# Kernel tuning notes

Hardware: AMD Instinct MI355X
Metric: run time of the kernel (lower is better)

## Reference

```python
import jax, jax.numpy as jnp
import numpy as np

N, P, E, HID = 20000, 12, 640000, 100

def setup_inputs() -> dict:
    key = jax.random.key(0)
    ks = jax.random.split(key, 20)
    inp = {}
    inp['x'] = jax.random.normal(ks[0], (N, P), dtype=jnp.float32)
    inp['edge_index'] = jax.random.randint(ks[1], (2, E), 0, N, dtype=jnp.int64)
    inp['edge_weight'] = jax.random.uniform(ks[2], (E,), dtype=jnp.float32)
    s = 0.1
    # GCNConv weights (in=1, out=HID) and biases for z, r, h gates
    inp['W_z'] = jax.random.normal(ks[3], (1, HID)) * s
    inp['b_z'] = jnp.zeros((HID,))
    inp['W_r'] = jax.random.normal(ks[4], (1, HID)) * s
    inp['b_r'] = jnp.zeros((HID,))
    inp['W_h'] = jax.random.normal(ks[5], (1, HID)) * s
    inp['b_h'] = jnp.zeros((HID,))
    # TGCN linear layers: Linear(2*HID, HID), stored as (in, out)
    inp['Wl_z'] = jax.random.normal(ks[6], (2 * HID, HID)) * s
    inp['bl_z'] = jnp.zeros((HID,))
    inp['Wl_r'] = jax.random.normal(ks[7], (2 * HID, HID)) * s
    inp['bl_r'] = jnp.zeros((HID,))
    inp['Wl_h'] = jax.random.normal(ks[8], (2 * HID, HID)) * s
    inp['bl_h'] = jnp.zeros((HID,))
    # A3TGCN temporal attention logits over periods
    inp['att'] = jax.random.uniform(ks[9], (P,))
    # final Linear(100, 1)
    inp['W_out'] = jax.random.normal(ks[10], (HID, 1)) * s
    inp['b_out'] = jnp.zeros((1,))
    return inp

def _gcn_aggregate(x_np, edge_index, edge_weight):
    # symmetric GCN normalization with self-loops (PyG gcn_norm), then
    # aggregate neighbor features: out[i] = sum_j norm_ij * x[j]
    n = x_np.shape[0]
    src, dst = edge_index[0], edge_index[1]
    loop = jnp.arange(n)
    s = jnp.concatenate([src, loop])
    d = jnp.concatenate([dst, loop])
    w = jnp.concatenate([edge_weight, jnp.ones((n,), dtype=x_np.dtype)])
    deg = jax.ops.segment_sum(w, d, num_segments=n)
    dinv = jnp.where(deg > 0, deg ** -0.5, 0.0)
    norm = dinv[s] * w * dinv[d]                      # (E+N,)
    msgs = norm[:, None] * x_np[s]                    # (E+N, P)
    return jax.ops.segment_sum(msgs, d, num_segments=n)  # (N, P)

def reference(x, edge_index, edge_weight, W_z, b_z, W_r, b_r, W_h, b_h,
              Wl_z, bl_z, Wl_r, bl_r, Wl_h, bl_h, att, W_out, b_out):
    # x: (N, P) -> viewed as (N, in_channels=1, P) in the torch module.
    # GCNConv is linear in x, so aggregate once and apply each gate's weight.
    agg = _gcn_aggregate(x, edge_index, edge_weight)       # (N, P)
    C_z = agg[:, :, None] * W_z[0] + b_z                   # (N, P, HID)
    C_r = agg[:, :, None] * W_r[0] + b_r
    C_h = agg[:, :, None] * W_h[0] + b_h
    # A3TGCN calls TGCN with H=None (zeros) for every period independently.
    H0 = jnp.zeros_like(C_z)
    Z = jax.nn.sigmoid(jnp.concatenate([C_z, H0], -1) @ Wl_z + bl_z)
    R = jax.nn.sigmoid(jnp.concatenate([C_r, H0], -1) @ Wl_r + bl_r)
    Ht = jnp.tanh(jnp.concatenate([C_h, H0 * R], -1) @ Wl_h + bl_h)
    Hp = Z * H0 + (1.0 - Z) * Ht                           # (N, P, HID)
    probs = jax.nn.softmax(att)                            # (P,)
    H_acc = jnp.einsum('npo,p->no', Hp, probs)             # (N, HID)
    h = jax.nn.relu(H_acc)
    return h @ W_out + b_out                               # (N, 1)
```

## Files before the change

kernel.cpp:

```cpp
#include <hip/hip_runtime.h>
#include <hip/hip_bf16.h>

constexpr int N_NODES = 20000;
constexpr int P_PER   = 12;
constexpr int N_EDGES = 640000;
constexpr int HID     = 100;

constexpr int BIN_W   = 64;
constexpr int NB      = (N_NODES + BIN_W - 1) / BIN_W;
constexpr int BCAP    = 2560;
constexpr int NBLK2   = 320;
constexpr int CHUNK   = N_EDGES / NBLK2;
constexpr int CUR_STR = 16;
constexpr int Y_STR   = 16;
constexpr int GL      = 8;

constexpr size_t OFF_DINV  = 0;
constexpr size_t OFF_UZ    = OFF_DINV + N_NODES;
constexpr size_t OFF_CZ    = OFF_UZ + HID;
constexpr size_t OFF_UH    = OFF_CZ + HID;
constexpr size_t OFF_CH    = OFF_UH + HID;
constexpr size_t OFF_PROBS = OFF_CH + HID;
constexpr size_t OFF_CUR   = 20416;
constexpr size_t OFF_Y     = OFF_CUR + (size_t)NB * CUR_STR;
constexpr size_t OFF_SEG   = OFF_Y + (size_t)N_NODES * Y_STR;
constexpr size_t OFF_SEG2  = OFF_SEG + (size_t)NB * BCAP * 2;
constexpr size_t OFF_ROW   = OFF_SEG2 + (size_t)NB * BCAP * 2;

__global__ __launch_bounds__(256) void precompute_kernel(
        const float* __restrict__ Wz, const float* __restrict__ bz,
        const float* __restrict__ Wh, const float* __restrict__ bh,
        const float* __restrict__ Wlz, const float* __restrict__ blz,
        const float* __restrict__ Wlh, const float* __restrict__ blh,
        const float* __restrict__ att,
        float* __restrict__ uz, float* __restrict__ cz,
        float* __restrict__ uh, float* __restrict__ ch,
        float* __restrict__ probs, int* __restrict__ cur) {
    int t = threadIdx.x;
    for (int i = t; i < NB * CUR_STR; i += 256) cur[i] = 0;
    if (t < HID) {
        float suz = 0.f, scz = 0.f, suh = 0.f, sch = 0.f;
        for (int j = 0; j < HID; ++j) {
            float wlz = Wlz[j * HID + t];
            float wlh = Wlh[j * HID + t];
            suz += Wz[j] * wlz;
            scz += bz[j] * wlz;
            suh += Wh[j] * wlh;
            sch += bh[j] * wlh;
        }
        uz[t] = suz;
        cz[t] = scz + blz[t];
        uh[t] = suh;
        ch[t] = sch + blh[t];
    }
    if (t == 0) {
        float m = att[0];
        for (int p = 1; p < P_PER; ++p) m = fmaxf(m, att[p]);
        float e[P_PER];
        float s = 0.f;
        for (int p = 0; p < P_PER; ++p) { e[p] = __expf(att[p] - m); s += e[p]; }
        float inv = 1.0f / s;
        for (int p = 0; p < P_PER; ++p) probs[p] = e[p] * inv;
    }
}

__global__ __launch_bounds__(256) void partition_kernel(const int* __restrict__ ei,
                                                        const float* __restrict__ w,
                                                        int* __restrict__ cur,
                                                        int2* __restrict__ seg) {
    __shared__ int hist[NB];
    __shared__ int base[NB];
    __shared__ int run[NB];
    int t = threadIdx.x;
    for (int b = t; b < NB; b += 256) { hist[b] = 0; run[b] = 0; }
    __syncthreads();
    int e0 = blockIdx.x * CHUNK;
    const int* __restrict__ dsts = ei + N_EDGES;
    for (int i = t; i < CHUNK; i += 256) {
        int d = dsts[e0 + i];
        atomicAdd(&hist[d >> 6], 1);
    }
    __syncthreads();
    for (int b = t; b < NB; b += 256) {
        int h = hist[b];
        base[b] = (h > 0) ? atomicAdd(cur + (size_t)b * CUR_STR, h) : 0;
    }
    __syncthreads();
    for (int i = t; i < CHUNK; i += 256) {
        int s = ei[e0 + i];
        int d = dsts[e0 + i];
        float wt = w[e0 + i];
        int b = d >> 6;
        int pos = base[b] + atomicAdd(&run[b], 1);
        if (pos < BCAP)
            seg[(size_t)b * BCAP + pos] = make_int2(s | ((d & 63) << 16), __float_as_int(wt));
    }
}

__global__ __launch_bounds__(256) void binsort_kernel(const int2* __restrict__ seg,
                                                      const int* __restrict__ cur,
                                                      const float* __restrict__ x,
                                                      float* __restrict__ y,
                                                      int2* __restrict__ seg2,
                                                      int4* __restrict__ rowinfo) {
    __shared__ int2 ent2[BCAP];
    __shared__ int  hist[BIN_W];
    __shared__ int  off[BIN_W];
    __shared__ int  excl[BIN_W];
    __shared__ float sdinv[BIN_W];
    int t = threadIdx.x;
    int b = blockIdx.x;
    if (t < BIN_W) hist[t] = 0;
    __syncthreads();
    int c = min(cur[(size_t)b * CUR_STR], BCAP);
    const int2* sg = seg + (size_t)b * BCAP;
    for (int i = t; i < c; i += 256) atomicAdd(&hist[sg[i].x >> 16], 1);
    __syncthreads();
    if (t < 64) {
        int v = hist[t];
        int inc = v;
#pragma unroll
        for (int o = 1; o < 64; o <<= 1) {
            int u = __shfl_up(inc, o, 64);
            if (t >= o) inc += u;
        }
        int ex = inc - v;
        excl[t] = ex;
        off[t]  = ex;
    }
    __syncthreads();
    for (int i = t; i < c; i += 256) {
        int2 e = sg[i];
        int dl = e.x >> 16;
        int p = atomicAdd(&off[dl], 1);
        ent2[p] = make_int2(e.x & 0xFFFF, e.y);
    }
    __syncthreads();
    {
        int nl = t >> 2, l = t & 3;
        int beg = excl[nl];
        int end = beg + hist[nl];
        float s = 0.f;
        for (int j = beg + l; j < end; j += 4) s += __int_as_float(ent2[j].y);
        s += __shfl_xor(s, 1, 64);
        s += __shfl_xor(s, 2, 64);
        if (l == 0) sdinv[nl] = rsqrtf(1.0f + s);
    }
    __syncthreads();
    int n0 = b * BIN_W;
    int2* s2 = seg2 + (size_t)b * BCAP;
    for (int i = t; i < c; i += 256) s2[i] = ent2[i];
    if (t < BIN_W && n0 + t < N_NODES)
        rowinfo[n0 + t] = make_int4(b * BCAP + excl[t], hist[t],
                                    __float_as_int(sdinv[t]), 0);
    for (int i = t; i < BIN_W * P_PER; i += 256) {
        int nl = i / P_PER, p = i - nl * P_PER;
        int n = n0 + nl;
        if (n < N_NODES) y[(size_t)n * Y_STR + p] = sdinv[nl] * x[(size_t)n * P_PER + p];
    }
}

__global__ __launch_bounds__(256) void gather_finalize_kernel(const int2* __restrict__ seg2,
                                                              const int4* __restrict__ rowinfo,
                                                              const float* __restrict__ y,
                                                              const float* __restrict__ uz,
                                                              const float* __restrict__ cz,
                                                              const float* __restrict__ uh,
                                                              const float* __restrict__ ch,
                                                              const float* __restrict__ probs,
                                                              const float* __restrict__ Wout,
                                                              const float* __restrict__ bout,
                                                              float* __restrict__ out) {
    __shared__ float s_uz[HID], s_cz[HID], s_uh[HID], s_ch[HID], s_wo[HID];
    __shared__ float s_pr[P_PER];
    int t = threadIdx.x;
    if (t < HID) {
        s_uz[t] = uz[t]; s_cz[t] = cz[t];
        s_uh[t] = uh[t]; s_ch[t] = ch[t];
        s_wo[t] = Wout[t];
    }
    if (t < P_PER) s_pr[t] = probs[t];
    __syncthreads();

    int tid = blockIdx.x * blockDim.x + t;
    int n = tid >> 3;
    int l = tid & (GL - 1);
    if (n >= N_NODES) return;

    int4 ri = rowinfo[n];
    float acc[P_PER];
#pragma unroll
    for (int p = 0; p < P_PER; ++p) acc[p] = 0.f;
    int end = ri.x + ri.y;
    for (int j = ri.x + l; j < end; j += GL) {
        int2 e = seg2[j];
        float wt = __int_as_float(e.y);
        const float4* yr = (const float4*)(y + (size_t)e.x * Y_STR);
        float4 y0 = yr[0], y1 = yr[1], y2 = yr[2];
        acc[0]  += wt * y0.x;  acc[1]  += wt * y0.y;
        acc[2]  += wt * y0.z;  acc[3]  += wt * y0.w;
        acc[4]  += wt * y1.x;  acc[5]  += wt * y1.y;
        acc[6]  += wt * y1.z;  acc[7]  += wt * y1.w;
        acc[8]  += wt * y2.x;  acc[9]  += wt * y2.y;
        acc[10] += wt * y2.z;  acc[11] += wt * y2.w;
    }
#pragma unroll
    for (int off = 4; off >= 1; off >>= 1) {
#pragma unroll
        for (int p = 0; p < P_PER; ++p) acc[p] += __shfl_xor(acc[p], off, 64);
    }
    {
        float dn = __int_as_float(ri.z);
        const float4* yr = (const float4*)(y + (size_t)n * Y_STR);
        float4 y0 = yr[0], y1 = yr[1], y2 = yr[2];
        acc[0]  = dn * (acc[0]  + y0.x);  acc[1]  = dn * (acc[1]  + y0.y);
        acc[2]  = dn * (acc[2]  + y0.z);  acc[3]  = dn * (acc[3]  + y0.w);
        acc[4]  = dn * (acc[4]  + y1.x);  acc[5]  = dn * (acc[5]  + y1.y);
        acc[6]  = dn * (acc[6]  + y1.z);  acc[7]  = dn * (acc[7]  + y1.w);
        acc[8]  = dn * (acc[8]  + y2.x);  acc[9]  = dn * (acc[9]  + y2.y);
        acc[10] = dn * (acc[10] + y2.z);  acc[11] = dn * (acc[11] + y2.w);
    }
    float rk = 0.f;
    for (int k = l; k < HID; k += GL) {
        float uzk = s_uz[k], czk = s_cz[k], uhk = s_uh[k], chk = s_ch[k];
        float a2 = 0.f;
#pragma unroll
        for (int p = 0; p < P_PER; ++p) {
            float av = acc[p];
            float vz = fminf(fmaxf(av * uzk + czk, -30.f), 30.f);
            float vh = fminf(fmaxf(av * uhk + chk, -15.f), 15.f);
            float ez  = __expf(vz);
            float e2h = __expf(2.0f * vh);
            float term = (e2h - 1.0f) / ((1.0f + ez) * (e2h + 1.0f));
            a2 += s_pr[p] * term;
        }
        rk += fmaxf(a2, 0.0f) * s_wo[k];
    }
#pragma unroll
    for (int off = 4; off >= 1; off >>= 1) rk += __shfl_xor(rk, off, 64);
    if (l == 0) out[n] = rk + bout[0];
}

extern "C" void kernel_launch(void* const* d_in, const int* in_sizes, int n_in,
                              void* d_out, int out_size, void* d_ws, size_t ws_size,
                              hipStream_t stream) {
    const float* x   = (const float*)d_in[0];
    const int*   ei  = (const int*)d_in[1];
    const float* ew  = (const float*)d_in[2];
    const float* Wz  = (const float*)d_in[3];
    const float* bz  = (const float*)d_in[4];
    const float* Wh  = (const float*)d_in[7];
    const float* bh  = (const float*)d_in[8];
    const float* Wlz = (const float*)d_in[9];
    const float* blz = (const float*)d_in[10];
    const float* Wlh = (const float*)d_in[13];
    const float* blh = (const float*)d_in[14];
    const float* att = (const float*)d_in[15];
    const float* Wout = (const float*)d_in[16];
    const float* bout = (const float*)d_in[17];
    float* out = (float*)d_out;

    float* ws      = (float*)d_ws;
    float* uz      = ws + OFF_UZ;
    float* cz      = ws + OFF_CZ;
    float* uh      = ws + OFF_UH;
    float* ch      = ws + OFF_CH;
    float* probs   = ws + OFF_PROBS;
    int*   cur     = (int*)(ws + OFF_CUR);
    float* y       = ws + OFF_Y;
    int2*  seg     = (int2*)(ws + OFF_SEG);
    int2*  seg2    = (int2*)(ws + OFF_SEG2);
    int4*  rowinfo = (int4*)(ws + OFF_ROW);

    hipLaunchKernelGGL(precompute_kernel, dim3(1), dim3(256), 0, stream,
                       Wz, bz, Wh, bh, Wlz, blz, Wlh, blh, att, uz, cz, uh, ch, probs, cur);
    hipLaunchKernelGGL(partition_kernel, dim3(NBLK2), dim3(256), 0, stream,
                       ei, ew, cur, seg);
    hipLaunchKernelGGL(binsort_kernel, dim3(NB), dim3(256), 0, stream,
                       seg, cur, x, y, seg2, rowinfo);
    hipLaunchKernelGGL(gather_finalize_kernel, dim3((N_NODES * GL + 255) / 256), dim3(256), 0, stream,
                       seg2, rowinfo, y, uz, cz, uh, ch, probs, Wout, bout, out);
}
```

Baseline: 157.4 us.

## Fuse partition, binsort and gather into one cooperative grid-synced kernel

```diff
diff --git a/kernel.cpp b/kernel.cpp
--- a/kernel.cpp
+++ b/kernel.cpp
@@ -1,199 +1,176 @@
 #include <hip/hip_runtime.h>
 #include <hip/hip_bf16.h>
+#include <hip/hip_cooperative_groups.h>
+
+namespace cg = cooperative_groups;
 
 constexpr int N_NODES = 20000;
 constexpr int P_PER   = 12;
 constexpr int N_EDGES = 640000;
 constexpr int HID     = 100;
 
-constexpr int BIN_W   = 64;
-constexpr int NB      = (N_NODES + BIN_W - 1) / BIN_W;
-constexpr int BCAP    = 2560;
-constexpr int NBLK2   = 320;
-constexpr int CHUNK   = N_EDGES / NBLK2;
-constexpr int CUR_STR = 16;
-constexpr int Y_STR   = 16;
-constexpr int GL      = 8;
-
-constexpr size_t OFF_DINV  = 0;
-constexpr size_t OFF_UZ    = OFF_DINV + N_NODES;
+constexpr int BIN_W  = 64;
+constexpr int NB     = (N_NODES + BIN_W - 1) / BIN_W;
+constexpr int GRID   = 512;
+constexpr int TPB    = 256;
+constexpr int PCHUNK = N_EDGES / GRID;
+constexpr int SCAP   = 20;
+constexpr int ECAP   = 2560;
+constexpr int Y_STR  = 16;
+
+constexpr size_t OFF_UZ    = 0;
 constexpr size_t OFF_CZ    = OFF_UZ + HID;
 constexpr size_t OFF_UH    = OFF_CZ + HID;
 constexpr size_t OFF_CH    = OFF_UH + HID;
 constexpr size_t OFF_PROBS = OFF_CH + HID;
-constexpr size_t OFF_CUR   = 20416;
-constexpr size_t OFF_Y     = OFF_CUR + (size_t)NB * CUR_STR;
+constexpr size_t OFF_COUNT = 416;
+constexpr size_t OFF_Y     = OFF_COUNT + (size_t)GRID * NB;
 constexpr size_t OFF_SEG   = OFF_Y + (size_t)N_NODES * Y_STR;
-constexpr size_t OFF_SEG2  = OFF_SEG + (size_t)NB * BCAP * 2;
-constexpr size_t OFF_ROW   = OFF_SEG2 + (size_t)NB * BCAP * 2;
-
-__global__ __launch_bounds__(256) void precompute_kernel(
+
+__global__ __launch_bounds__(TPB) void fused_kernel(
+        const float* __restrict__ x, const int* __restrict__ ei, const float* __restrict__ ew,
         const float* __restrict__ Wz, const float* __restrict__ bz,
         const float* __restrict__ Wh, const float* __restrict__ bh,
         const float* __restrict__ Wlz, const float* __restrict__ blz,
         const float* __restrict__ Wlh, const float* __restrict__ blh,
-        const float* __restrict__ att,
-        float* __restrict__ uz, float* __restrict__ cz,
-        float* __restrict__ uh, float* __restrict__ ch,
-        float* __restrict__ probs, int* __restrict__ cur) {
-    int t = threadIdx.x;
-    for (int i = t; i < NB * CUR_STR; i += 256) cur[i] = 0;
-    if (t < HID) {
-        float suz = 0.f, scz = 0.f, suh = 0.f, sch = 0.f;
-        for (int j = 0; j < HID; ++j) {
-            float wlz = Wlz[j * HID + t];
-            float wlh = Wlh[j * HID + t];
-            suz += Wz[j] * wlz;
-            scz += bz[j] * wlz;
-            suh += Wh[j] * wlh;
-            sch += bh[j] * wlh;
-        }
-        uz[t] = suz;
-        cz[t] = scz + blz[t];
-        uh[t] = suh;
-        ch[t] = sch + blh[t];
-    }
-    if (t == 0) {
-        float m = att[0];
-        for (int p = 1; p < P_PER; ++p) m = fmaxf(m, att[p]);
-        float e[P_PER];
-        float s = 0.f;
-        for (int p = 0; p < P_PER; ++p) { e[p] = __expf(att[p] - m); s += e[p]; }
-        float inv = 1.0f / s;
-        for (int p = 0; p < P_PER; ++p) probs[p] = e[p] * inv;
-    }
-}
-
-__global__ __launch_bounds__(256) void partition_kernel(const int* __restrict__ ei,
-                                                        const float* __restrict__ w,
-                                                        int* __restrict__ cur,
-                                                        int2* __restrict__ seg) {
-    __shared__ int hist[NB];
-    __shared__ int base[NB];
-    __shared__ int run[NB];
-    int t = threadIdx.x;
-    for (int b = t; b < NB; b += 256) { hist[b] = 0; run[b] = 0; }
-    __syncthreads();
-    int e0 = blockIdx.x * CHUNK;
-    const int* __restrict__ dsts = ei + N_EDGES;
-    for (int i = t; i < CHUNK; i += 256) {
-        int d = dsts[e0 + i];
-        atomicAdd(&hist[d >> 6], 1);
-    }
-    __syncthreads();
-    for (int b = t; b < NB; b += 256) {
-        int h = hist[b];
-        base[b] = (h > 0) ? atomicAdd(cur + (size_t)b * CUR_STR, h) : 0;
-    }
-    __syncthreads();
-    for (int i = t; i < CHUNK; i += 256) {
-        int s = ei[e0 + i];
-        int d = dsts[e0 + i];
-        float wt = w[e0 + i];
-        int b = d >> 6;
-        int pos = base[b] + atomicAdd(&run[b], 1);
-        if (pos < BCAP)
-            seg[(size_t)b * BCAP + pos] = make_int2(s | ((d & 63) << 16), __float_as_int(wt));
-    }
-}
-
-__global__ __launch_bounds__(256) void binsort_kernel(const int2* __restrict__ seg,
-                                                      const int* __restrict__ cur,
-                                                      const float* __restrict__ x,
-                                                      float* __restrict__ y,
-                                                      int2* __restrict__ seg2,
-                                                      int4* __restrict__ rowinfo) {
-    __shared__ int2 ent2[BCAP];
-    __shared__ int  hist[BIN_W];
-    __shared__ int  off[BIN_W];
-    __shared__ int  excl[BIN_W];
+        const float* __restrict__ att, const float* __restrict__ Wout,
+        const float* __restrict__ bout, float* __restrict__ out,
+        float* __restrict__ uzg, float* __restrict__ czg,
+        float* __restrict__ uhg, float* __restrict__ chg, float* __restrict__ probsg,
+        int* __restrict__ count, float* __restrict__ y, int2* __restrict__ seg) {
+    cg::grid_group grid = cg::this_grid();
+
+    __shared__ int   run[NB];
+    __shared__ int   scnt[GRID];
+    __shared__ int2  ent2[ECAP];
+    __shared__ int   nhist[BIN_W], nexcl[BIN_W], noff[BIN_W];
     __shared__ float sdinv[BIN_W];
-    int t = threadIdx.x;
-    int b = blockIdx.x;
-    if (t < BIN_W) hist[t] = 0;
-    __syncthreads();
-    int c = min(cur[(size_t)b * CUR_STR], BCAP);
-    const int2* sg = seg + (size_t)b * BCAP;
-    for (int i = t; i < c; i += 256) atomicAdd(&hist[sg[i].x >> 16], 1);
-    __syncthreads();
-    if (t < 64) {
-        int v = hist[t];
-        int inc = v;
-#pragma unroll
-        for (int o = 1; o < 64; o <<= 1) {
-            int u = __shfl_up(inc, o, 64);
-            if (t >= o) inc += u;
-        }
-        int ex = inc - v;
-        excl[t] = ex;
-        off[t]  = ex;
-    }
-    __syncthreads();
-    for (int i = t; i < c; i += 256) {
-        int2 e = sg[i];
-        int dl = e.x >> 16;
-        int p = atomicAdd(&off[dl], 1);
-        ent2[p] = make_int2(e.x & 0xFFFF, e.y);
-    }
+    __shared__ float s_uz[HID], s_cz[HID], s_uh[HID], s_ch[HID], s_wo[HID];
+    __shared__ float s_pr[P_PER];
+
+    const int t   = threadIdx.x;
+    const int blk = blockIdx.x;
+
+    for (int b = t; b < NB; b += TPB) run[b] = 0;
     __syncthreads();
     {
-        int nl = t >> 2, l = t & 3;
-        int beg = excl[nl];
-        int end = beg + hist[nl];
-        float s = 0.f;
-        for (int j = beg + l; j < end; j += 4) s += __int_as_float(ent2[j].y);
-        s += __shfl_xor(s, 1, 64);
-        s += __shfl_xor(s, 2, 64);
-        if (l == 0) sdinv[nl] = rsqrtf(1.0f + s);
+        const int e0 = blk * PCHUNK;
+        const int* __restrict__ dsts = ei + N_EDGES;
+        for (int i = t; i < PCHUNK; i += TPB) {
+            int d = dsts[e0 + i];
+            int s = ei[e0 + i];
+            float wt = ew[e0 + i];
+            int j = d >> 6;
+            int slot = atomicAdd(&run[j], 1);
+            if (slot < SCAP)
+                seg[((size_t)j * GRID + blk) * SCAP + slot] =
+                    make_int2(s | ((d & 63) << 16), __float_as_int(wt));
+        }
     }
     __syncthreads();
-    int n0 = b * BIN_W;
-    int2* s2 = seg2 + (size_t)b * BCAP;
-    for (int i = t; i < c; i += 256) s2[i] = ent2[i];
-    if (t < BIN_W && n0 + t < N_NODES)
-        rowinfo[n0 + t] = make_int4(b * BCAP + excl[t], hist[t],
-                                    __float_as_int(sdinv[t]), 0);
-    for (int i = t; i < BIN_W * P_PER; i += 256) {
-        int nl = i / P_PER, p = i - nl * P_PER;
-        int n = n0 + nl;
-        if (n < N_NODES) y[(size_t)n * Y_STR + p] = sdinv[nl] * x[(size_t)n * P_PER + p];
-    }
-}
-
-__global__ __launch_bounds__(256) void gather_finalize_kernel(const int2* __restrict__ seg2,
-                                                              const int4* __restrict__ rowinfo,
-                                                              const float* __restrict__ y,
-                                                              const float* __restrict__ uz,
-                                                              const float* __restrict__ cz,
-                                                              const float* __restrict__ uh,
-                                                              const float* __restrict__ ch,
-                                                              const float* __restrict__ probs,
-                                                              const float* __restrict__ Wout,
-                                                              const float* __restrict__ bout,
-                                                              float* __restrict__ out) {
-    __shared__ float s_uz[HID], s_cz[HID], s_uh[HID], s_ch[HID], s_wo[HID];
-    __shared__ float s_pr[P_PER];
-    int t = threadIdx.x;
+    for (int b = t; b < NB; b += TPB) count[blk * NB + b] = min(run[b], SCAP);
+
+    grid.sync();
+
+    if (blk == GRID - 1) {
+        if (t < HID) {
+            float suz = 0.f, scz = 0.f, suh = 0.f, sch = 0.f;
+            for (int j = 0; j < HID; ++j) {
+                float wlz = Wlz[j * HID + t];
+                float wlh = Wlh[j * HID + t];
+                suz += Wz[j] * wlz;
+                scz += bz[j] * wlz;
+                suh += Wh[j] * wlh;
+                sch += bh[j] * wlh;
+            }
+            uzg[t] = suz;
+            czg[t] = scz + blz[t];
+            uhg[t] = suh;
+            chg[t] = sch + blh[t];
+        }
+        if (t == 0) {
+            float m = att[0];
+            for (int p = 1; p < P_PER; ++p) m = fmaxf(m, att[p]);
+            float e[P_PER];
+            float s = 0.f;
+            for (int p = 0; p < P_PER; ++p) { e[p] = __expf(att[p] - m); s += e[p]; }
+            float inv = 1.0f / s;
+            for (int p = 0; p < P_PER; ++p) probsg[p] = e[p] * inv;
+        }
+    } else if (blk < NB) {
+        const int j = blk;
+        for (int i = t; i < GRID; i += TPB) scnt[i] = count[i * NB + j];
+        if (t < BIN_W) nhist[t] = 0;
+        __syncthreads();
+        for (int i = t; i < GRID; i += TPB) {
+            int cnt = scnt[i];
+            const int2* sp = seg + ((size_t)j * GRID + i) * SCAP;
+            for (int k = 0; k < cnt; ++k) atomicAdd(&nhist[sp[k].x >> 16], 1);
+        }
+        __syncthreads();
+        if (t < 64) {
+            int v = nhist[t];
+            int inc = v;
+#pragma unroll
+            for (int o = 1; o < 64; o <<= 1) {
+                int u = __shfl_up(inc, o, 64);
+                if (t >= o) inc += u;
+            }
+            nexcl[t] = inc - v;
+            noff[t]  = inc - v;
+        }
+        __syncthreads();
+        for (int i = t; i < GRID; i += TPB) {
+            int cnt = scnt[i];
+            const int2* sp = seg + ((size_t)j * GRID + i) * SCAP;
+            for (int k = 0; k < cnt; ++k) {
+                int2 e = sp[k];
+                int dl = e.x >> 16;
+                int p = atomicAdd(&noff[dl], 1);
+                if (p < ECAP) ent2[p] = make_int2(e.x & 0xFFFF, e.y);
+            }
+        }
+        __syncthreads();
+        {
+            int nl = t >> 2, l = t & 3;
+            int beg = nexcl[nl], len = nhist[nl];
+            float s = 0.f;
+            for (int q = beg + l; q < beg + len; q += 4) s += __int_as_float(ent2[q].y);
+            s += __shfl_xor(s, 1, 64);
+            s += __shfl_xor(s, 2, 64);
+            if (l == 0) sdinv[nl] = rsqrtf(1.0f + s);
+        }
+        __syncthreads();
+        int n0 = j * BIN_W;
+        for (int i = t; i < BIN_W * P_PER; i += TPB) {
+            int nl = i / P_PER, p = i - nl * P_PER;
+            int n = n0 + nl;
+            if (n < N_NODES) y[(size_t)n * Y_STR + p] = sdinv[nl] * x[(size_t)n * P_PER + p];
+        }
+    }
+
+    grid.sync();
+
+    if (blk >= NB) return;
     if (t < HID) {
-        s_uz[t] = uz[t]; s_cz[t] = cz[t];
-        s_uh[t] = uh[t]; s_ch[t] = ch[t];
+        s_uz[t] = uzg[t]; s_cz[t] = czg[t];
+        s_uh[t] = uhg[t]; s_ch[t] = chg[t];
         s_wo[t] = Wout[t];
     }
-    if (t < P_PER) s_pr[t] = probs[t];
+    if (t < P_PER) s_pr[t] = probsg[t];
     __syncthreads();
 
-    int tid = blockIdx.x * blockDim.x + t;
-    int n = tid >> 3;
-    int l = tid & (GL - 1);
+    int nl = t >> 2;
+    int l  = t & 3;
+    int n  = blk * BIN_W + nl;
     if (n >= N_NODES) return;
 
-    int4 ri = rowinfo[n];
+    int beg = nexcl[nl], len = nhist[nl];
     float acc[P_PER];
 #pragma unroll
     for (int p = 0; p < P_PER; ++p) acc[p] = 0.f;
-    int end = ri.x + ri.y;
-    for (int j = ri.x + l; j < end; j += GL) {
-        int2 e = seg2[j];
+    for (int q = beg + l; q < beg + len; q += 4) {
+        int2 e = ent2[q];
         float wt = __int_as_float(e.y);
         const float4* yr = (const float4*)(y + (size_t)e.x * Y_STR);
         float4 y0 = yr[0], y1 = yr[1], y2 = yr[2];
@@ -205,12 +182,12 @@
         acc[10] += wt * y2.z;  acc[11] += wt * y2.w;
     }
 #pragma unroll
-    for (int off = 4; off >= 1; off >>= 1) {
+    for (int off = 1; off <= 2; off <<= 1) {
 #pragma unroll
         for (int p = 0; p < P_PER; ++p) acc[p] += __shfl_xor(acc[p], off, 64);
     }
     {
-        float dn = __int_as_float(ri.z);
+        float dn = sdinv[nl];
         const float4* yr = (const float4*)(y + (size_t)n * Y_STR);
         float4 y0 = yr[0], y1 = yr[1], y2 = yr[2];
         acc[0]  = dn * (acc[0]  + y0.x);  acc[1]  = dn * (acc[1]  + y0.y);
@@ -221,7 +198,7 @@
         acc[10] = dn * (acc[10] + y2.z);  acc[11] = dn * (acc[11] + y2.w);
     }
     float rk = 0.f;
-    for (int k = l; k < HID; k += GL) {
+    for (int k = l; k < HID; k += 4) {
         float uzk = s_uz[k], czk = s_cz[k], uhk = s_uh[k], chk = s_ch[k];
         float a2 = 0.f;
 #pragma unroll
@@ -236,8 +213,8 @@
         }
         rk += fmaxf(a2, 0.0f) * s_wo[k];
     }
-#pragma unroll
-    for (int off = 4; off >= 1; off >>= 1) rk += __shfl_xor(rk, off, 64);
+    rk += __shfl_xor(rk, 1, 64);
+    rk += __shfl_xor(rk, 2, 64);
     if (l == 0) out[n] = rk + bout[0];
 }
 
@@ -260,24 +237,24 @@
     const float* bout = (const float*)d_in[17];
     float* out = (float*)d_out;
 
-    float* ws      = (float*)d_ws;
-    float* uz      = ws + OFF_UZ;
-    float* cz      = ws + OFF_CZ;
-    float* uh      = ws + OFF_UH;
-    float* ch      = ws + OFF_CH;
-    float* probs   = ws + OFF_PROBS;
-    int*   cur     = (int*)(ws + OFF_CUR);
-    float* y       = ws + OFF_Y;
-    int2*  seg     = (int2*)(ws + OFF_SEG);
-    int2*  seg2    = (int2*)(ws + OFF_SEG2);
-    int4*  rowinfo = (int4*)(ws + OFF_ROW);
-
-    hipLaunchKernelGGL(precompute_kernel, dim3(1), dim3(256), 0, stream,
-                       Wz, bz, Wh, bh, Wlz, blz, Wlh, blh, att, uz, cz, uh, ch, probs, cur);
-    hipLaunchKernelGGL(partition_kernel, dim3(NBLK2), dim3(256), 0, stream,
-                       ei, ew, cur, seg);
-    hipLaunchKernelGGL(binsort_kernel, dim3(NB), dim3(256), 0, stream,
-                       seg, cur, x, y, seg2, rowinfo);
-    hipLaunchKernelGGL(gather_finalize_kernel, dim3((N_NODES * GL + 255) / 256), dim3(256), 0, stream,
-                       seg2, rowinfo, y, uz, cz, uh, ch, probs, Wout, bout, out);
+    float* ws     = (float*)d_ws;
+    float* uzg    = ws + OFF_UZ;
+    float* czg    = ws + OFF_CZ;
+    float* uhg    = ws + OFF_UH;
+    float* chg    = ws + OFF_CH;
+    float* probsg = ws + OFF_PROBS;
+    int*   count  = (int*)(ws + OFF_COUNT);
+    float* y      = ws + OFF_Y;
+    int2*  seg    = (int2*)(ws + OFF_SEG);
+
+    void* args[] = {
+        (void*)&x, (void*)&ei, (void*)&ew,
+        (void*)&Wz, (void*)&bz, (void*)&Wh, (void*)&bh,
+        (void*)&Wlz, (void*)&blz, (void*)&Wlh, (void*)&blh,
+        (void*)&att, (void*)&Wout, (void*)&bout, (void*)&out,
+        (void*)&uzg, (void*)&czg, (void*)&uhg, (void*)&chg, (void*)&probsg,
+        (void*)&count, (void*)&y, (void*)&seg
+    };
+    hipLaunchCooperativeKernel((const void*)fused_kernel, dim3(GRID), dim3(TPB),
+                               args, 0, stream);
 }
```

Measured after the change: 298.9 us. +89.8%, slower.
